# Kernel tuning notes

Measured on AMD Instinct MI355X. Metric: run time of the kernel, lower is better.

The kernel has to match this reference:

```python
import jax, jax.numpy as jnp
import numpy as np
from jax import lax

P = 32      # AR order
D = 1       # differencing order (d=1 -> inverse_difference is last_value + ar_term)
Q = 1       # MA order (only used via max(p, q) threshold)
EPS = 1e-5  # RevIN eps


def setup_inputs() -> dict:
    key = jax.random.key(0)
    k1, k2, k3 = jax.random.split(key, 3)
    S = 1048576
    y = jax.random.normal(k1, (1, S, 1), dtype=jnp.float32)
    ar_weight = jax.random.normal(k2, (1, P), dtype=jnp.float32) * 0.1
    ar_bias = jax.random.normal(k3, (1,), dtype=jnp.float32) * 0.1
    rev_weight = jnp.ones((1,), dtype=jnp.float32)
    rev_bias = jnp.zeros((1,), dtype=jnp.float32)
    return {"y": y, "ar_weight": ar_weight, "ar_bias": ar_bias,
            "rev_weight": rev_weight, "rev_bias": rev_bias}


def reference(y, ar_weight, ar_bias, rev_weight, rev_bias):
    # Vectorized form of ARIMA.mse_loss for B=1, C=1 (as the torch code requires).
    S = y.shape[1]
    yf = y[0, :, 0]                                  # (S,)
    t0 = max(P, Q) + 1                               # first t where `t > max(p, q)` holds
    T = S - t0                                       # number of predicted timesteps
    # Sliding windows: for t = t0 + i, window = y[t-P : t]
    idx = (t0 - P) + jnp.arange(T)[:, None] + jnp.arange(P)[None, :]
    win = yf[idx]                                    # (T, P)
    # RevIN 'norm' (statistics are detached in torch)
    mean = lax.stop_gradient(jnp.mean(win, axis=1, keepdims=True))          # (T, 1)
    std = lax.stop_gradient(jnp.sqrt(jnp.var(win, axis=1, keepdims=True) + EPS))
    norm = (win - mean) / std * rev_weight[0] + rev_bias[0]                 # (T, P)
    # difference (d = 1): keep first value, first differences after
    dser = jnp.concatenate([norm[:, :1], norm[:, 1:] - norm[:, :-1]], axis=1)
    # AR term: Linear(P, 1) on the flattened diffed window
    ar = dser @ ar_weight[0] + ar_bias[0]            # (T,)
    # inverse_difference with d=1: last diffed value + cumsum(single step) = last + ar
    pred_d = dser[:, -1] + ar                        # (T,)
    # RevIN 'denorm'
    pred = (pred_d - rev_bias[0]) / (rev_weight[0] + EPS * EPS) * std[:, 0] + mean[:, 0]
    # errors: zero prediction for t <= max(p, q)
    err_pred = yf[t0:] - pred
    loss = (jnp.sum(yf[:t0] ** 2) + jnp.sum(err_pred ** 2)) / S
    return loss
```

## Files before the change

kernel.cpp:

```cpp
#include <hip/hip_runtime.h>


#define PP   32
#define T0V  33
#define BLK  256

__global__ __launch_bounds__(BLK) void arima_main(
    const float* __restrict__ y, const float* __restrict__ arw,
    const float* __restrict__ arb, const float* __restrict__ rvw,
    const float* __restrict__ rvb, float* __restrict__ partial,
    int S, int T)
{
    __shared__ float sh[BLK + PP];
    __shared__ float wsh[PP];
    __shared__ float red[BLK / 64];

    const int tid  = threadIdx.x;
    const int base = blockIdx.x * BLK;

    int gi = 1 + base + tid;
    sh[tid] = (gi < S) ? y[gi] : 0.0f;
    if (tid < PP) {
        int gi2 = gi + BLK;
        sh[BLK + tid] = (gi2 < S) ? y[gi2] : 0.0f;
        wsh[tid] = arw[tid];
    }
    __syncthreads();

    const float rw   = rvw[0];
    const float rb   = rvb[0];
    const float bias = arb[0];

    const int t = base + tid;
    float val = 0.0f;
    if (t < T) {
        float s = 0.0f;
        #pragma unroll
        for (int j = 0; j < PP; ++j) s += sh[tid + j];
        const float mean = s * (1.0f / PP);

        float v = 0.0f;
        #pragma unroll
        for (int j = 0; j < PP; ++j) { float d = sh[tid + j] - mean; v += d * d; }
        const float stdv  = sqrtf(v * (1.0f / PP) + 1e-5f);
        const float scale = rw / stdv;

        float acc  = bias;
        float prev = 0.0f, prev2 = 0.0f;
        #pragma unroll
        for (int j = 0; j < PP; ++j) {
            float nj = (sh[tid + j] - mean) * scale + rb;
            float d  = (j == 0) ? nj : (nj - prev);
            acc += d * wsh[j];
            prev2 = prev;
            prev  = nj;
        }
        const float pred_d = (prev - prev2) + acc;
        const float pred   = (pred_d - rb) / (rw + 1e-10f) * stdv + mean;
        const float err    = sh[tid + PP] - pred;
        val = err * err;
    }

    #pragma unroll
    for (int o = 32; o > 0; o >>= 1) val += __shfl_down(val, o, 64);
    if ((tid & 63) == 0) red[tid >> 6] = val;
    __syncthreads();
    if (tid == 0) partial[blockIdx.x] = red[0] + red[1] + red[2] + red[3];
}

__global__ __launch_bounds__(BLK) void arima_finish(
    const float* __restrict__ partial, int nblocks,
    const float* __restrict__ y, float* __restrict__ out, int S)
{
    __shared__ float red[BLK / 64];
    const int tid = threadIdx.x;

    float s = 0.0f;
    for (int i = tid; i < nblocks; i += BLK) s += partial[i];
    #pragma unroll
    for (int o = 32; o > 0; o >>= 1) s += __shfl_down(s, o, 64);
    if ((tid & 63) == 0) red[tid >> 6] = s;
    __syncthreads();

    if (tid == 0) {
        float tot = red[0] + red[1] + red[2] + red[3];
        float head = 0.0f;
        for (int i = 0; i < T0V; ++i) { float v = y[i]; head += v * v; }
        out[0] = (tot + head) / (float)S;
    }
}

extern "C" void kernel_launch(void* const* d_in, const int* in_sizes, int n_in,
                              void* d_out, int out_size, void* d_ws, size_t ws_size,
                              hipStream_t stream)
{
    const float* y   = (const float*)d_in[0];
    const float* arw = (const float*)d_in[1];
    const float* arb = (const float*)d_in[2];
    const float* rvw = (const float*)d_in[3];
    const float* rvb = (const float*)d_in[4];
    float* out       = (float*)d_out;
    float* partial   = (float*)d_ws;

    const int S = in_sizes[0];
    const int T = S - T0V;
    const int nblocks = (T + BLK - 1) / BLK;

    arima_main<<<nblocks, BLK, 0, stream>>>(y, arw, arb, rvw, rvb, partial, S, T);
    arima_finish<<<1, BLK, 0, stream>>>(partial, nblocks, y, out, S);
}
```

Before: 72.83 us.

## Fold RevIN/difference algebra into precomputed weights and process 8 windows per thread

Rewrites the per-window computation algebraically: the normalize-difference-linear-denormalize chain collapses into a single dot product of raw values with differenced weights plus mean/std correction terms. Mean and variance come from running sums that slide across 8 consecutive windows per thread. Inputs are loaded as float4 into registers instead of shared memory. The head-sum work moves into the main kernel. This cuts per-element arithmetic and synchronisation, but the E[x^2]-mean^2 variance is less numerically stable and register pressure rises.

```diff
diff --git a/kernel.cpp b/kernel.cpp
--- a/kernel.cpp
+++ b/kernel.cpp
@@ -4,61 +4,76 @@
 #define PP   32
 #define T0V  33
 #define BLK  256
+#define RW   8
+#define SPAN (RW + 36)
 
-__global__ __launch_bounds__(BLK) void arima_main(
+__global__ __launch_bounds__(BLK, 2) void arima_main(
     const float* __restrict__ y, const float* __restrict__ arw,
     const float* __restrict__ arb, const float* __restrict__ rvw,
     const float* __restrict__ rvb, float* __restrict__ partial,
     int S, int T)
 {
-    __shared__ float sh[BLK + PP];
-    __shared__ float wsh[PP];
     __shared__ float red[BLK / 64];
 
-    const int tid  = threadIdx.x;
-    const int base = blockIdx.x * BLK;
+    const int tid = threadIdx.x;
+    const int gt0 = (blockIdx.x * BLK + tid) * RW;
 
-    int gi = 1 + base + tid;
-    sh[tid] = (gi < S) ? y[gi] : 0.0f;
-    if (tid < PP) {
-        int gi2 = gi + BLK;
-        sh[BLK + tid] = (gi2 < S) ? y[gi2] : 0.0f;
-        wsh[tid] = arw[tid];
+    float xs[SPAN];
+    #pragma unroll
+    for (int k = 0; k < SPAN; k += 4) {
+        const int gi = gt0 + k;
+        if (gi + 3 < S) {
+            const float4 v = *reinterpret_cast<const float4*>(y + gi);
+            xs[k] = v.x; xs[k + 1] = v.y; xs[k + 2] = v.z; xs[k + 3] = v.w;
+        } else {
+            xs[k]     = (gi     < S) ? y[gi]     : 0.0f;
+            xs[k + 1] = (gi + 1 < S) ? y[gi + 1] : 0.0f;
+            xs[k + 2] = (gi + 2 < S) ? y[gi + 2] : 0.0f;
+            xs[k + 3] = (gi + 3 < S) ? y[gi + 3] : 0.0f;
+        }
     }
-    __syncthreads();
 
     const float rw   = rvw[0];
     const float rb   = rvb[0];
     const float bias = arb[0];
+    const float w0   = arw[0];
+    const float C2   = (rb * (w0 - 1.0f) + bias) / (rw + 1e-10f);
 
-    const int t = base + tid;
+    float c[PP];
+    #pragma unroll
+    for (int j = 0; j < PP; ++j)
+        c[j] = arw[j] - ((j < PP - 1) ? arw[j + 1] : 0.0f);
+
+    float s1 = 0.0f, s2 = 0.0f;
+    #pragma unroll
+    for (int k = 1; k <= PP; ++k) { const float x = xs[k]; s1 += x; s2 = fmaf(x, x, s2); }
+
     float val = 0.0f;
-    if (t < T) {
-        float s = 0.0f;
-        #pragma unroll
-        for (int j = 0; j < PP; ++j) s += sh[tid + j];
-        const float mean = s * (1.0f / PP);
+    #pragma unroll
+    for (int r = 0; r < RW; ++r) {
+        if (r > 0) {
+            const float xo = xs[r], xn = xs[r + PP];
+            s1 += xn - xo;
+            s2 = fmaf(xn, xn, fmaf(-xo, xo, s2));
+        }
+        if (gt0 + r < T) {
+            float a = 0.0f;
+            #pragma unroll
+            for (int j = 0; j < PP; ++j) a = fmaf(xs[r + 1 + j], c[j], a);
 
-        float v = 0.0f;
-        #pragma unroll
-        for (int j = 0; j < PP; ++j) { float d = sh[tid + j] - mean; v += d * d; }
-        const float stdv  = sqrtf(v * (1.0f / PP) + 1e-5f);
-        const float scale = rw / stdv;
+            const float mean = s1 * (1.0f / PP);
+            const float varp = fmaf(-mean, mean, s2 * (1.0f / PP));
+            const float stdv = sqrtf(varp + 1e-5f);
+            const float dlast = xs[r + PP] - xs[r + PP - 1];
+            const float pred = a - mean * w0 + dlast + C2 * stdv + mean;
+            const float err  = xs[r + PP + 1] - pred;
+            val = fmaf(err, err, val);
+        }
+    }
 
-        float acc  = bias;
-        float prev = 0.0f, prev2 = 0.0f;
-        #pragma unroll
-        for (int j = 0; j < PP; ++j) {
-            float nj = (sh[tid + j] - mean) * scale + rb;
-            float d  = (j == 0) ? nj : (nj - prev);
-            acc += d * wsh[j];
-            prev2 = prev;
-            prev  = nj;
-        }
-        const float pred_d = (prev - prev2) + acc;
-        const float pred   = (pred_d - rb) / (rw + 1e-10f) * stdv + mean;
-        const float err    = sh[tid + PP] - pred;
-        val = err * err;
+    if (blockIdx.x == 0 && tid < T0V) {
+        const float h = y[tid];
+        val = fmaf(h, h, val);
     }
 
     #pragma unroll
@@ -70,7 +85,7 @@
 
 __global__ __launch_bounds__(BLK) void arima_finish(
     const float* __restrict__ partial, int nblocks,
-    const float* __restrict__ y, float* __restrict__ out, int S)
+    float* __restrict__ out, float invS)
 {
     __shared__ float red[BLK / 64];
     const int tid = threadIdx.x;
@@ -81,13 +96,7 @@
     for (int o = 32; o > 0; o >>= 1) s += __shfl_down(s, o, 64);
     if ((tid & 63) == 0) red[tid >> 6] = s;
     __syncthreads();
-
-    if (tid == 0) {
-        float tot = red[0] + red[1] + red[2] + red[3];
-        float head = 0.0f;
-        for (int i = 0; i < T0V; ++i) { float v = y[i]; head += v * v; }
-        out[0] = (tot + head) / (float)S;
-    }
+    if (tid == 0) out[0] = (red[0] + red[1] + red[2] + red[3]) * invS;
 }
 
 extern "C" void kernel_launch(void* const* d_in, const int* in_sizes, int n_in,
@@ -104,8 +113,9 @@
 
     const int S = in_sizes[0];
     const int T = S - T0V;
-    const int nblocks = (T + BLK - 1) / BLK;
+    const int per_block = BLK * RW;
+    const int nblocks = (T + per_block - 1) / per_block;
 
     arima_main<<<nblocks, BLK, 0, stream>>>(y, arw, arb, rvw, rvb, partial, S, T);
-    arima_finish<<<1, BLK, 0, stream>>>(partial, nblocks, y, out, S);
+    arima_finish<<<1, BLK, 0, stream>>>(partial, nblocks, out, 1.0f / (float)S);
 }
```

Result: faster. 66.41 us (-8.8%).
